# Kernel tuning notes

Measured on AMD Instinct MI355X. Metric: run time of the kernel, lower is better.

## Reference

```python
import jax, jax.numpy as jnp
import numpy as np

CROP = 48
THRESHOLD = 0.5
IOU_THRESHOLD = 0.5


def _conv(x, w, b):
    # x: [N,H,W,C], w: [kh,kw,Cin,Cout]
    y = jax.lax.conv_general_dilated(x, w, (1, 1), 'VALID',
                                     dimension_numbers=('NHWC', 'HWIO', 'NHWC'))
    return y + b


def _prelu(x, a):
    # a broadcasts over the channel-last axis
    return jnp.where(x >= 0, x, a * x)


def _maxpool(x, k, s, p):
    return jax.lax.reduce_window(x, -jnp.inf, jax.lax.max,
                                 (1, k, k, 1), (1, s, s, 1),
                                 ((0, 0), (p, p), (p, p), (0, 0)))


def _nms_keep(boxes, scores, valid, iou_thr):
    # fixed-shape greedy NMS (torchvision semantics: suppress iou > thr)
    N = boxes.shape[0]
    s = jnp.where(valid, scores, -jnp.inf)
    order = jnp.argsort(-s)
    b = boxes[order]
    x1, y1, x2, y2 = b[:, 0], b[:, 1], b[:, 2], b[:, 3]
    area = (x2 - x1) * (y2 - y1)
    xx1 = jnp.maximum(x1[:, None], x1[None, :])
    yy1 = jnp.maximum(y1[:, None], y1[None, :])
    xx2 = jnp.minimum(x2[:, None], x2[None, :])
    yy2 = jnp.minimum(y2[:, None], y2[None, :])
    inter = jnp.clip(xx2 - xx1, 0.0) * jnp.clip(yy2 - yy1, 0.0)
    iou = inter / (area[:, None] + area[None, :] - inter + 1e-12)
    keep0 = valid[order]
    idx = jnp.arange(N)

    def body(i, keep):
        sup = (iou[i] > iou_thr) & (idx > i) & keep[i] & keep
        return keep & ~sup

    keep_sorted = jax.lax.fori_loop(0, N, body, keep0)
    return jnp.zeros(N, bool).at[order].set(keep_sorted)


def setup_inputs() -> dict:
    key = jax.random.key(0)
    ks = jax.random.split(key, 24)
    H = W = 1024
    N = 2048
    image = jax.random.uniform(ks[0], (H, W, 3), jnp.float32) * 255.0
    x1 = jax.random.uniform(ks[1], (N,), jnp.float32) * (W - 130)
    y1 = jax.random.uniform(ks[2], (N,), jnp.float32) * (H - 130)
    bw = 20.0 + jax.random.uniform(ks[3], (N,), jnp.float32) * 100.0
    bh = 20.0 + jax.random.uniform(ks[4], (N,), jnp.float32) * 100.0
    bboxes = jnp.stack([x1, y1, x1 + bw, y1 + bh], axis=1)
    rn = lambda k, sh, s: jax.random.normal(k, sh, jnp.float32) * s
    return {
        'bboxes': bboxes, 'image': image,
        'conv1_w': rn(ks[5], (3, 3, 3, 32), 0.05), 'conv1_b': rn(ks[6], (32,), 0.01),
        'prelu1': 0.25 * jnp.ones((32,), jnp.float32),
        'conv2_w': rn(ks[7], (3, 3, 32, 64), 0.05), 'conv2_b': rn(ks[8], (64,), 0.01),
        'prelu2': 0.25 * jnp.ones((64,), jnp.float32),
        'conv3_w': rn(ks[9], (3, 3, 64, 64), 0.05), 'conv3_b': rn(ks[10], (64,), 0.01),
        'prelu3': 0.25 * jnp.ones((64,), jnp.float32),
        'conv4_w': rn(ks[11], (2, 2, 64, 128), 0.05), 'conv4_b': rn(ks[12], (128,), 0.01),
        'prelu4': 0.25 * jnp.ones((128,), jnp.float32),
        'fc5_w': rn(ks[13], (256, 1152), 0.02), 'fc5_b': rn(ks[14], (256,), 0.01),
        'prelu5': 0.25 * jnp.ones((256,), jnp.float32),
        'fc6a_w': rn(ks[15], (2, 256), 0.1), 'fc6a_b': rn(ks[16], (2,), 0.01),
        'fc6b_w': rn(ks[17], (4, 256), 0.1), 'fc6b_b': rn(ks[18], (4,), 0.01),
    }


def reference(bboxes, image, conv1_w, conv1_b, prelu1, conv2_w, conv2_b, prelu2,
              conv3_w, conv3_b, prelu3, conv4_w, conv4_b, prelu4,
              fc5_w, fc5_b, prelu5, fc6a_w, fc6a_b, fc6b_w, fc6b_b):
    H, W = image.shape[0], image.shape[1]
    N = bboxes.shape[0]
    # preprocess (torch: (x - 127.5) * 0.0078125)
    data = (image - 127.5) * 0.0078125  # [H,W,3]
    # clip boxes in place like the torch forward
    bx1 = jnp.clip(bboxes[:, 0], 0.0, None)
    by1 = jnp.clip(bboxes[:, 1], 0.0, None)
    bx2 = jnp.clip(bboxes[:, 2], None, float(W))
    by2 = jnp.clip(bboxes[:, 3], None, float(H))
    bb = jnp.stack([bx1, by1, bx2, by2], axis=1)  # clipped boxes [N,4]
    # integer crop windows (torch .int() truncation; coords >= 0)
    ib = bb.astype(jnp.int32)
    cw = jnp.maximum(ib[:, 2] - ib[:, 0], 1)
    ch = jnp.maximum(ib[:, 3] - ib[:, 1], 1)
    # nearest-neighbor resize to 48x48 (F.interpolate default mode='nearest')
    r = jnp.arange(CROP, dtype=jnp.int32)
    xs = ib[:, 0:1] + (r[None, :] * cw[:, None]) // CROP  # [N,48]
    ys = ib[:, 1:2] + (r[None, :] * ch[:, None]) // CROP  # [N,48]
    crops = data[ys[:, :, None], xs[:, None, :], :]  # [N,48,48,3] gather
    # CNN trunk
    h = _maxpool(_prelu(_conv(crops, conv1_w, conv1_b), prelu1), 3, 2, 1)
    h = _maxpool(_prelu(_conv(h, conv2_w, conv2_b), prelu2), 3, 2, 0)
    h = _maxpool(_prelu(_conv(h, conv3_w, conv3_b), prelu3), 2, 2, 0)
    h = _prelu(_conv(h, conv4_w, conv4_b), prelu4)  # [N,3,3,128]
    h = jnp.transpose(h, (0, 3, 1, 2)).reshape(N, -1)  # NCHW flatten like torch -> [N,1152]
    h = _prelu(h @ fc5_w.T + fc5_b, prelu5)  # [N,256]
    cls = jax.nn.softmax(h @ fc6a_w.T + fc6a_b, axis=1)  # [N,2]
    reg = h @ fc6b_w.T + fc6b_b  # [N,4]
    score = cls[:, 1]
    valid = score >= THRESHOLD
    w = bb[:, 2] - bb[:, 0]
    hgt = bb[:, 3] - bb[:, 1]
    out = jnp.stack([bb[:, 0] + reg[:, 0] * w,
                     bb[:, 1] + reg[:, 1] * hgt,
                     bb[:, 2] + reg[:, 2] * w,
                     bb[:, 3] + reg[:, 3] * hgt], axis=1)  # [N,4]
    keep = _nms_keep(out, score, valid, IOU_THRESHOLD)
    return jnp.where(keep[:, None], out, 0.0)
```

## Files before the change

### kernel.cpp

```cpp
#include <hip/hip_runtime.h>
#include <math.h>
#include <stdint.h>

#define NBOX 2048

#define P1_RS 25
#define P1_CS 576
#define P1_SZ 18432

__device__ __forceinline__ void fma4(float4& a, float s, const float4& w) {
  a.x = fmaf(s, w.x, a.x); a.y = fmaf(s, w.y, a.y);
  a.z = fmaf(s, w.z, a.z); a.w = fmaf(s, w.w, a.w);
}
__device__ __forceinline__ float4 max4(float4 a, float4 b) {
  return make_float4(fmaxf(a.x,b.x), fmaxf(a.y,b.y), fmaxf(a.z,b.z), fmaxf(a.w,b.w));
}
__device__ __forceinline__ float4 max34(float4 a, float4 b, float4 c) {
  return max4(max4(a, b), c);
}
__device__ __forceinline__ float4 prelu4(float4 v, float4 a) {
  float4 r;
  r.x = v.x >= 0.f ? v.x : a.x*v.x;
  r.y = v.y >= 0.f ? v.y : a.y*v.y;
  r.z = v.z >= 0.f ? v.z : a.z*v.z;
  r.w = v.w >= 0.f ? v.w : a.w*v.w;
  return r;
}
__device__ __forceinline__ float4 shfl4(float4 v, int src) {
  float4 r;
  r.x = __shfl(v.x, src, 64); r.y = __shfl(v.y, src, 64);
  r.z = __shfl(v.z, src, 64); r.w = __shfl(v.w, src, 64);
  return r;
}

__global__ __launch_bounds__(256) void k1_crop_conv1(
    const float* __restrict__ bboxes, const float* __restrict__ image,
    const float* __restrict__ w1, const float* __restrict__ b1, const float* __restrict__ a1,
    float* __restrict__ p1ws, int box0)
{
  __shared__ float crop[48*48*3];
  __shared__ float w1s[27*32];
  __shared__ float b1s[32], a1s[32];
  const int tid = threadIdx.x;
  const int n = box0 + blockIdx.x;

  for (int idx = tid; idx < 27*32; idx += 256) w1s[idx] = w1[idx];
  if (tid < 32) { b1s[tid] = b1[tid]; a1s[tid] = a1[tid]; }

  float f0 = bboxes[n*4+0], f1 = bboxes[n*4+1], f2 = bboxes[n*4+2], f3 = bboxes[n*4+3];
  float bx1 = fmaxf(f0, 0.f), by1 = fmaxf(f1, 0.f);
  float bx2 = fminf(f2, 1024.f), by2 = fminf(f3, 1024.f);
  int ix1 = (int)bx1, iy1 = (int)by1, ix2 = (int)bx2, iy2 = (int)by2;
  int cw = ix2 - ix1; if (cw < 1) cw = 1;
  int ch = iy2 - iy1; if (ch < 1) ch = 1;

  for (int idx = tid; idx < 6912; idx += 256) {
    int c = idx % 3; int t = idx / 3; int j = t % 48; int i = t / 48;
    int gx = ix1 + (j * cw) / 48;
    int gy = iy1 + (i * ch) / 48;
    float v = image[(gy*1024 + gx)*3 + c];
    crop[idx] = (v - 127.5f) * 0.0078125f;
  }
  __syncthreads();

  float* p1o = p1ws + (size_t)blockIdx.x * P1_SZ;

  for (int slot = tid; slot < 1104; slot += 256) {
    int cq = slot & 7;
    int t2 = slot >> 3;
    int pjq = t2 % 6;
    int pi  = t2 / 6;
    int pj0 = pjq * 4;
    int c0 = 2*pj0 - 1;
    float4 bias  = *(const float4*)&b1s[cq*4];
    float4 alpha = *(const float4*)&a1s[cq*4];
    float4 mx[4];
#pragma unroll
    for (int t = 0; t < 4; t++) mx[t] = make_float4(-3.0e38f,-3.0e38f,-3.0e38f,-3.0e38f);

#pragma unroll
    for (int dr = 0; dr < 3; dr++) {
      int r = 2*pi - 1 + dr;
      if (r < 0 || r > 45) continue;
      float4 acc[9];
#pragma unroll
      for (int c = 0; c < 9; c++) acc[c] = bias;
#pragma unroll
      for (int kh = 0; kh < 3; kh++) {
        int row = r + kh;
        float s[33];
#pragma unroll
        for (int d = 0; d < 11; d++) {
          int cc = c0 + d; cc = cc < 0 ? 0 : (cc > 47 ? 47 : cc);
          int base = row*144 + cc*3;
          s[d*3+0] = crop[base+0];
          s[d*3+1] = crop[base+1];
          s[d*3+2] = crop[base+2];
        }
#pragma unroll
        for (int kw = 0; kw < 3; kw++) {
#pragma unroll
          for (int ci = 0; ci < 3; ci++) {
            float4 w = *(const float4*)&w1s[((kh*3+kw)*3+ci)*32 + cq*4];
#pragma unroll
            for (int c = 0; c < 9; c++) fma4(acc[c], s[(c+kw)*3+ci], w);
          }
        }
      }
#pragma unroll
      for (int c = 0; c < 9; c++) {
        int cabs = c0 + c;
        if (cabs < 0 || cabs > 45) continue;
        float4 pv = prelu4(acc[c], alpha);
#pragma unroll
        for (int t = 0; t < 4; t++) {
          if (c >= 2*t && c <= 2*t+2) mx[t] = max4(mx[t], pv);
        }
      }
    }
#pragma unroll
    for (int t = 0; t < 4; t++) {
      int pj = pj0 + t;
      if (pj < 23) {
        int base = pi*P1_RS + pj;
        p1o[(cq*4+0)*P1_CS + base] = mx[t].x;
        p1o[(cq*4+1)*P1_CS + base] = mx[t].y;
        p1o[(cq*4+2)*P1_CS + base] = mx[t].z;
        p1o[(cq*4+3)*P1_CS + base] = mx[t].w;
      }
    }
  }
}

#define K2_LOADW(W, CI, KH) { \
  const float* wp_ = w2 + (((KH)*3)*32 + (CI))*64 + co0; \
  W[0] = *(const float4*)(wp_);            W[1] = *(const float4*)(wp_ + 4); \
  W[2] = *(const float4*)(wp_ + 2048);     W[3] = *(const float4*)(wp_ + 2052); \
  W[4] = *(const float4*)(wp_ + 4096);     W[5] = *(const float4*)(wp_ + 4100); }

#define K2_COMP(W, CIL, KH) { \
  const float* ip_ = &in_s[(CIL)*P1_CS + (rl+(KH))*P1_RS + j0]; \
  float s_[9]; \
  _Pragma("unroll") for (int d_ = 0; d_ < 9; d_++) s_[d_] = ip_[d_]; \
  _Pragma("unroll") for (int kw_ = 0; kw_ < 3; kw_++) { \
    _Pragma("unroll") for (int jj_ = 0; jj_ < 7; jj_++) { \
      fma4(acc[jj_][0], s_[jj_+kw_], W[kw_*2]); \
      fma4(acc[jj_][1], s_[jj_+kw_], W[kw_*2+1]); } } }

#define K2_STORE8(PJ, LO, HI) { \
  float* d_ = p2o + (size_t)co0*120 + pi*12 + (PJ); \
  float4 lo_ = (LO), hi_ = (HI); \
  d_[0]   = lo_.x; d_[120] = lo_.y; d_[240] = lo_.z; d_[360] = lo_.w; \
  d_[480] = hi_.x; d_[600] = hi_.y; d_[720] = hi_.z; d_[840] = hi_.w; }

__global__ __launch_bounds__(512, 4) void k2_conv2(
    const float* __restrict__ w2, const float* __restrict__ b2, const float* __restrict__ a2,
    const float* __restrict__ p1ws, float* __restrict__ p2ws)
{
  __shared__ float in_s[9216];
  const int tid = threadIdx.x;
  const float* p1o = p1ws + (size_t)blockIdx.x * P1_SZ;
  float* p2o = p2ws + (size_t)blockIdx.x * 7680;

  const int wav = __builtin_amdgcn_readfirstlane(tid >> 6);
  const int lane = tid & 63;
  int jt = lane / 21;
  int rl = lane - jt * 21;
  if (lane == 63) { jt = 2; rl = 20; }
  const int j0 = jt * 7;
  const int co0 = wav * 8;

  float4 bL = *(const float4*)&b2[co0];
  float4 bH = *(const float4*)&b2[co0+4];
  float4 aL = *(const float4*)&a2[co0];
  float4 aH = *(const float4*)&a2[co0+4];

  float4 acc[7][2];
#pragma unroll
  for (int jj = 0; jj < 7; jj++) { acc[jj][0] = bL; acc[jj][1] = bH; }

#pragma unroll 1
  for (int h = 0; h < 2; h++) {
    __syncthreads();
    for (int i4 = tid; i4 < 2304; i4 += 512)
      *(float4*)&in_s[i4*4] = *(const float4*)&p1o[h*9216 + i4*4];
    __syncthreads();

    const int cb = h*16;
    float4 wA[6], wB[6];
    K2_LOADW(wA, cb+0, 0);
#pragma unroll 1
    for (int ci = 0; ci < 16; ci += 2) {
      K2_LOADW(wB, cb+ci, 1);
      K2_COMP(wA, ci, 0);
      K2_LOADW(wA, cb+ci, 2);
      K2_COMP(wB, ci, 1);
      K2_LOADW(wB, cb+ci+1, 0);
      K2_COMP(wA, ci, 2);
      K2_LOADW(wA, cb+ci+1, 1);
      K2_COMP(wB, ci+1, 0);
      K2_LOADW(wB, cb+ci+1, 2);
      K2_COMP(wA, ci+1, 1);
      if (ci + 2 < 16) K2_LOADW(wA, cb+ci+2, 0);
      K2_COMP(wB, ci+1, 2);
    }
  }

#pragma unroll
  for (int jj = 0; jj < 7; jj++) {
    acc[jj][0] = prelu4(acc[jj][0], aL);
    acc[jj][1] = prelu4(acc[jj][1], aH);
  }

#pragma unroll
  for (int jj = 0; jj < 7; jj++) {
#pragma unroll
    for (int h = 0; h < 2; h++) {
      float4 v = acc[jj][h];
      float4 d1 = shfl4(v, lane + 1);
      float4 d2 = shfl4(v, lane + 2);
      acc[jj][h] = max34(v, d1, d2);
    }
  }
  float4 r0[2], r1[2];
#pragma unroll
  for (int h = 0; h < 2; h++) {
    r0[h] = shfl4(acc[0][h], lane + 21);
    r1[h] = shfl4(acc[1][h], lane + 21);
  }

  if (((rl & 1) == 0) && rl <= 18) {
    const int pi = rl >> 1;
    if (jt == 0) {
      K2_STORE8(0, max34(acc[0][0],acc[1][0],acc[2][0]), max34(acc[0][1],acc[1][1],acc[2][1]));
      K2_STORE8(1, max34(acc[2][0],acc[3][0],acc[4][0]), max34(acc[2][1],acc[3][1],acc[4][1]));
      K2_STORE8(2, max34(acc[4][0],acc[5][0],acc[6][0]), max34(acc[4][1],acc[5][1],acc[6][1]));
      K2_STORE8(3, max34(acc[6][0],r0[0],r1[0]),          max34(acc[6][1],r0[1],r1[1]));
    } else if (jt == 1) {
      K2_STORE8(4, max34(acc[1][0],acc[2][0],acc[3][0]), max34(acc[1][1],acc[2][1],acc[3][1]));
      K2_STORE8(5, max34(acc[3][0],acc[4][0],acc[5][0]), max34(acc[3][1],acc[4][1],acc[5][1]));
      K2_STORE8(6, max34(acc[5][0],acc[6][0],r0[0]),     max34(acc[5][1],acc[6][1],r0[1]));
    } else {
      K2_STORE8(7, max34(acc[0][0],acc[1][0],acc[2][0]), max34(acc[0][1],acc[1][1],acc[2][1]));
      K2_STORE8(8, max34(acc[2][0],acc[3][0],acc[4][0]), max34(acc[2][1],acc[3][1],acc[4][1]));
      K2_STORE8(9, max34(acc[4][0],acc[5][0],acc[6][0]), max34(acc[4][1],acc[5][1],acc[6][1]));
    }
  }
}

#define K3_LOADW(W, CI, KH) { \
  const float* wp_ = w3 + (((KH)*3)*64 + (CI))*64 + co0; \
  W[0] = *(const float4*)(wp_);            W[1] = *(const float4*)(wp_ + 4); \
  W[2] = *(const float4*)(wp_ + 4096);     W[3] = *(const float4*)(wp_ + 4100); \
  W[4] = *(const float4*)(wp_ + 8192);     W[5] = *(const float4*)(wp_ + 8196); }

#define K3_COMP(W, CIL, KH) { \
  const float* ip_ = ibase + (CIL)*120 + (KH)*12; \
  float2 sA_ = *(const float2*)(ip_); \
  float2 sB_ = *(const float2*)(ip_ + 2); \
  float s_[4] = {sA_.x, sA_.y, sB_.x, sB_.y}; \
  _Pragma("unroll") for (int kw_ = 0; kw_ < 3; kw_++) { \
    _Pragma("unroll") for (int c_ = 0; c_ < 2; c_++) { \
      fma4(acc[c_][0], s_[c_+kw_], W[kw_*2]); \
      fma4(acc[c_][1], s_[c_+kw_], W[kw_*2+1]); } } }

__global__ __launch_bounds__(512, 4) void k3_conv3(
    const float* __restrict__ w3, const float* __restrict__ b3, const float* __restrict__ a3,
    const float* __restrict__ p2ws, float* __restrict__ p3ws)
{
  __shared__ float in_s[7696];
  const int tid = threadIdx.x;
  const float* p2o = p2ws + (size_t)(blockIdx.x*2) * 7680;
  float* p3o0 = p3ws + (size_t)(blockIdx.x*2) * 1024;

  const int wav = __builtin_amdgcn_readfirstlane(tid >> 6);
  const int lane = tid & 63;
  const int b  = lane >> 5;
  const int r  = (lane >> 2) & 7;
  const int cg = lane & 3;
  const int co0 = wav * 8;

  float4 bL = *(const float4*)&b3[co0];
  float4 bH = *(const float4*)&b3[co0+4];
  float4 aL = *(const float4*)&a3[co0];
  float4 aH = *(const float4*)&a3[co0+4];

  float4 acc[2][2];
  acc[0][0] = bL; acc[0][1] = bH; acc[1][0] = bL; acc[1][1] = bH;

  const float* ibase = &in_s[b*3848 + r*12 + cg*2];

#pragma unroll 1
  for (int h = 0; h < 2; h++) {
    __syncthreads();
    for (int i4 = tid; i4 < 1920; i4 += 512) {
      int bb = (i4 >= 960) ? 1 : 0;
      int k = i4 - bb*960;
      *(float4*)&in_s[bb*3848 + k*4] = *(const float4*)&p2o[(size_t)bb*7680 + h*3840 + k*4];
    }
    __syncthreads();

    const int cb = h*32;
    float4 wA[6], wB[6];
    K3_LOADW(wA, cb+0, 0);
#pragma unroll 1
    for (int ci = 0; ci < 32; ci += 2) {
      K3_LOADW(wB, cb+ci, 1);
      K3_COMP(wA, ci, 0);
      K3_LOADW(wA, cb+ci, 2);
      K3_COMP(wB, ci, 1);
      K3_LOADW(wB, cb+ci+1, 0);
      K3_COMP(wA, ci, 2);
      K3_LOADW(wA, cb+ci+1, 1);
      K3_COMP(wB, ci+1, 0);
      K3_LOADW(wB, cb+ci+1, 2);
      K3_COMP(wA, ci+1, 1);
      if (ci + 2 < 32) K3_LOADW(wA, cb+ci+2, 0);
      K3_COMP(wB, ci+1, 2);
    }
  }

  float4 hm[2];
#pragma unroll
  for (int h = 0; h < 2; h++) {
    float4 p0 = prelu4(acc[0][h], h ? aH : aL);
    float4 p1 = prelu4(acc[1][h], h ? aH : aL);
    hm[h] = max4(p0, p1);
  }
  float4 o[2];
#pragma unroll
  for (int h = 0; h < 2; h++) {
    float4 d = shfl4(hm[h], lane + 4);
    o[h] = max4(hm[h], d);
  }
  if ((r & 1) == 0) {
    const int pi = r >> 1;
    float* d = p3o0 + b*1024 + (size_t)co0*16 + pi*4 + cg;
    d[0]   = o[0].x; d[16]  = o[0].y; d[32]  = o[0].z; d[48]  = o[0].w;
    d[64]  = o[1].x; d[80]  = o[1].y; d[96]  = o[1].z; d[112] = o[1].w;
  }
}

#define K4_LOADW(W, CI) { \
  const float* wp_ = w4 + (CI)*128 + co0; \
  W[0] = *(const float4*)(wp_);           W[1] = *(const float4*)(wp_ + 4); \
  W[2] = *(const float4*)(wp_ + 8192);    W[3] = *(const float4*)(wp_ + 8196); \
  W[4] = *(const float4*)(wp_ + 16384);   W[5] = *(const float4*)(wp_ + 16388); \
  W[6] = *(const float4*)(wp_ + 24576);   W[7] = *(const float4*)(wp_ + 24580); }

#define K4_COMP(W, CI) { \
  const float* ip_ = base + (CI)*16; \
  float i00 = ip_[0], i01 = ip_[1], i10 = ip_[4], i11 = ip_[5]; \
  fma4(acc0, i00, W[0]); fma4(acc1, i00, W[1]); \
  fma4(acc0, i01, W[2]); fma4(acc1, i01, W[3]); \
  fma4(acc0, i10, W[4]); fma4(acc1, i10, W[5]); \
  fma4(acc0, i11, W[6]); fma4(acc1, i11, W[7]); }

__global__ __launch_bounds__(512) void k4_conv4(
    const float* __restrict__ w4, const float* __restrict__ b4, const float* __restrict__ a4,
    const float* __restrict__ p3ws, float* __restrict__ c4ws)
{
  __shared__ float p3s[4*1032];
  const int tid = threadIdx.x;
  const int bi0 = blockIdx.x * 4;

  for (int i4 = tid; i4 < 1024; i4 += 512) {
    int bb = i4 >> 8, k = i4 & 255;
    *(float4*)&p3s[bb*1032 + k*4] = *(const float4*)&p3ws[(size_t)(bi0+bb)*1024 + k*4];
  }
  __syncthreads();

  const int wav = __builtin_amdgcn_readfirstlane(tid >> 6);
  const int lane = tid & 63;
  const int bx = lane >> 4;
  const int sp = lane & 15;
  const bool act = sp < 9;
  const int sq = act ? sp : 8;
  const int r = sq / 3, c = sq - 3*r;
  const float* base = &p3s[bx*1032 + r*4 + c];
  float* c4o = c4ws + (size_t)(bi0+bx)*1152;

#pragma unroll 1
  for (int p = 0; p < 2; p++) {
    const int co0 = p*64 + wav*8;
    float4 bL = *(const float4*)&b4[co0];
    float4 bH = *(const float4*)&b4[co0+4];
    float4 aL = *(const float4*)&a4[co0];
    float4 aH = *(const float4*)&a4[co0+4];
    float4 acc0 = bL, acc1 = bH;

    float4 wA[8], wB[8];
    K4_LOADW(wA, 0);
#pragma unroll 1
    for (int ci = 0; ci < 64; ci += 2) {
      K4_LOADW(wB, ci+1);
      K4_COMP(wA, ci);
      if (ci + 2 < 64) K4_LOADW(wA, ci+2);
      K4_COMP(wB, ci+1);
    }

    if (act) {
      float4 p0 = prelu4(acc0, aL);
      float4 p1 = prelu4(acc1, aH);
      float* d = c4o + (size_t)co0*9 + sp;
      d[0]  = p0.x; d[9]  = p0.y; d[18] = p0.z; d[27] = p0.w;
      d[36] = p1.x; d[45] = p1.y; d[54] = p1.z; d[63] = p1.w;
    }
  }
}

__global__ __launch_bounds__(256) void k5_fc(
    const float* __restrict__ fc5w, const float* __restrict__ fc5b, const float* __restrict__ a5,
    const float* __restrict__ w6a, const float* __restrict__ b6a,
    const float* __restrict__ w6b, const float* __restrict__ b6b,
    const float* __restrict__ bboxes, const float* __restrict__ c4ws,
    float* __restrict__ ws_scores, float* __restrict__ ws_boxes, int box0)
{
  __shared__ float c4s[8*1152];
  __shared__ float hs[8*256];
  __shared__ float l6[8][6];
  __shared__ float b5s[256], a5s[256];
  const int tid = threadIdx.x;
  const int lb0 = blockIdx.x * 8;
  b5s[tid] = fc5b[tid]; a5s[tid] = a5[tid];
  for (int idx4 = tid; idx4 < 2304; idx4 += 256)
    *(float4*)&c4s[idx4*4] = *(const float4*)&c4ws[(size_t)lb0*1152 + idx4*4];
  __syncthreads();

  const int og = tid & 31, bl = tid >> 5;
  float acc[8] = {0,0,0,0,0,0,0,0};
  const float* cbase = &c4s[bl*1152];
  for (int k = 0; k < 1152; k += 4) {
    float4 a = *(const float4*)&cbase[k];
#pragma unroll
    for (int u = 0; u < 8; u++) {
      int o = og + 32*u;
      float4 w = *(const float4*)&fc5w[(size_t)o*1152 + k];
      acc[u] += a.x*w.x + a.y*w.y + a.z*w.z + a.w*w.w;
    }
  }
#pragma unroll
  for (int u = 0; u < 8; u++) {
    int o = og + 32*u;
    float h = acc[u] + b5s[o];
    h = h >= 0.f ? h : a5s[o]*h;
    hs[bl*256 + o] = h;
  }
  __syncthreads();
  if (tid < 48) {
    int b = tid / 6, oi = tid % 6;
    const float* w = (oi < 2) ? &w6a[oi*256] : &w6b[(oi-2)*256];
    float d = (oi < 2) ? b6a[oi] : b6b[oi-2];
    const float* hh = &hs[b*256];
    for (int k = 0; k < 256; k++) d += hh[k]*w[k];
    l6[b][oi] = d;
  }
  __syncthreads();
  if (tid < 8) {
    int n = box0 + lb0 + tid;
    float l0 = l6[tid][0], l1 = l6[tid][1];
    float m = fmaxf(l0, l1);
    float e0 = expf(l0-m), e1 = expf(l1-m);
    float score = e1/(e0+e1);
    float r0 = l6[tid][2], r1 = l6[tid][3], r2 = l6[tid][4], r3 = l6[tid][5];
    float f0 = bboxes[n*4+0], f1 = bboxes[n*4+1], f2 = bboxes[n*4+2], f3 = bboxes[n*4+3];
    float bx1 = fmaxf(f0, 0.f), by1 = fmaxf(f1, 0.f);
    float bx2 = fminf(f2, 1024.f), by2 = fminf(f3, 1024.f);
    float w_ = bx2-bx1, h_ = by2-by1;
    ws_scores[n] = score;
    float4 ob = make_float4(bx1 + r0*w_, by1 + r1*h_, bx2 + r2*w_, by2 + r3*h_);
    *(float4*)&ws_boxes[n*4] = ob;
  }
}

__global__ __launch_bounds__(1024) void k6a_sort(
    const float* __restrict__ ws_scores, const float* __restrict__ ws_boxes,
    int* __restrict__ sidx_ws, float* __restrict__ sbox_ws,
    float* __restrict__ area_ws, int* __restrict__ nv_ws)
{
  __shared__ float skey[2048];
  __shared__ int   sidx[2048];
  const int tid = threadIdx.x;
  for (int i = tid; i < 2048; i += 1024) {
    float s = ws_scores[i];
    skey[i] = (s >= 0.5f) ? s : -INFINITY;
    sidx[i] = i;
  }
  __syncthreads();
  for (int k = 2; k <= 2048; k <<= 1) {
    for (int j = k >> 1; j > 0; j >>= 1) {
      for (int i = tid; i < 2048; i += 1024) {
        int ixj = i ^ j;
        if (ixj > i) {
          float a = skey[i], b = skey[ixj];
          int ia = sidx[i], ib = sidx[ixj];
          bool up = ((i & k) == 0);
          bool aAfterB = (a < b) || (a == b && ia > ib);
          if (up ? aAfterB : !aAfterB) {
            skey[i] = b; skey[ixj] = a; sidx[i] = ib; sidx[ixj] = ia;
          }
        }
      }
      __syncthreads();
    }
  }
  if (tid == 0) nv_ws[0] = 2048;
  __syncthreads();
  for (int i = tid; i < 2048; i += 1024) {
    if (skey[i] == -INFINITY && (i == 0 || skey[i-1] != -INFINITY)) nv_ws[0] = i;
    int n = sidx[i];
    sidx_ws[i] = n;
    float4 b = *(const float4*)&ws_boxes[n*4];
    *(float4*)&sbox_ws[i*4] = b;
    area_ws[i] = (b.z-b.x)*(b.w-b.y);
  }
}

__global__ __launch_bounds__(256) void k6b_iou(
    const int* __restrict__ nv_ws, const float* __restrict__ sbox_ws,
    const float* __restrict__ area_ws, unsigned long long* __restrict__ M)
{
  const int nv = nv_ws[0];
  int gt = blockIdx.x*256 + threadIdx.x;
  for (int w = gt; w < 2048*32; w += 128*256) {
    int i = w >> 5, wg = w & 31;
    if (i >= nv) continue;
    float4 bi = *(const float4*)&sbox_ws[i*4];
    float ai = area_ws[i];
    unsigned long long m = 0;
    int jbase = wg*64;
    if (jbase + 63 > i) {
      for (int jj = 0; jj < 64; jj++) {
        int j = jbase + jj;
        if (j <= i) continue;
        float4 bj = *(const float4*)&sbox_ws[j*4];
        float xx1 = fmaxf(bi.x, bj.x), yy1 = fmaxf(bi.y, bj.y);
        float xx2 = fminf(bi.z, bj.z), yy2 = fminf(bi.w, bj.w);
        float iw = fmaxf(xx2-xx1, 0.f), ih = fmaxf(yy2-yy1, 0.f);
        float inter = iw*ih;
        float iou = inter / (ai + area_ws[j] - inter + 1e-12f);
        if (iou > 0.5f) m |= (1ull << jj);
      }
    }
    M[w] = m;
  }
}

__global__ __launch_bounds__(1024) void k6c_scan(
    const int* __restrict__ nv_ws, const int* __restrict__ sidx_ws,
    const float* __restrict__ sbox_ws, const unsigned long long* __restrict__ M,
    float* __restrict__ out)
{
  __shared__ unsigned long long Msh[128*32];
  __shared__ unsigned long long rem_sh[32];
  const int tid = threadIdx.x;
  const int nv = nv_ws[0];
  unsigned long long rem = 0;

  for (int c0 = 0; c0 < 2048; c0 += 128) {
    if (c0 >= nv) break;
    for (int w = tid; w < 128*32; w += 1024) {
      int i = c0 + (w >> 5);
      if (i < nv) Msh[w] = M[(size_t)i*32 + (w & 31)];
    }
    __syncthreads();
    if (tid < 64) {
      int iend = c0 + 128; if (iend > nv) iend = nv;
      for (int i = c0; i < iend; i += 4) {
        unsigned long long m0=0, m1=0, m2=0, m3=0;
        int base = (i - c0) << 5;
        if (tid < 32) {
          m0 = Msh[base + tid];
          if (i+1 < iend) m1 = Msh[base + 32 + tid];
          if (i+2 < iend) m2 = Msh[base + 64 + tid];
          if (i+3 < iend) m3 = Msh[base + 96 + tid];
        }
        unsigned long long rw = __shfl(rem, (i >> 6), 64);
        if (!((rw >> (i & 63)) & 1ull)) rem |= m0;
        if (i+1 < iend) {
          rw = __shfl(rem, ((i+1) >> 6), 64);
          if (!((rw >> ((i+1) & 63)) & 1ull)) rem |= m1;
        }
        if (i+2 < iend) {
          rw = __shfl(rem, ((i+2) >> 6), 64);
          if (!((rw >> ((i+2) & 63)) & 1ull)) rem |= m2;
        }
        if (i+3 < iend) {
          rw = __shfl(rem, ((i+3) >> 6), 64);
          if (!((rw >> ((i+3) & 63)) & 1ull)) rem |= m3;
        }
      }
    }
    __syncthreads();
  }
  if (tid < 32) rem_sh[tid] = rem;
  __syncthreads();
  for (int i = tid; i < 2048; i += 1024) {
    bool keep = (i < nv) && !((rem_sh[i >> 6] >> (i & 63)) & 1ull);
    int n = sidx_ws[i];
    float4 b = *(const float4*)&sbox_ws[i*4];
    float4 o = keep ? b : make_float4(0.f,0.f,0.f,0.f);
    *(float4*)&out[n*4] = o;
  }
}

extern "C" void kernel_launch(void* const* d_in, const int* in_sizes, int n_in,
                              void* d_out, int out_size, void* d_ws, size_t ws_size,
                              hipStream_t stream)
{
  const float* bboxes = (const float*)d_in[0];
  const float* image  = (const float*)d_in[1];
  const float* w1 = (const float*)d_in[2];  const float* b1 = (const float*)d_in[3];  const float* a1 = (const float*)d_in[4];
  const float* w2 = (const float*)d_in[5];  const float* b2 = (const float*)d_in[6];  const float* a2 = (const float*)d_in[7];
  const float* w3 = (const float*)d_in[8];  const float* b3 = (const float*)d_in[9];  const float* a3 = (const float*)d_in[10];
  const float* w4 = (const float*)d_in[11]; const float* b4 = (const float*)d_in[12]; const float* a4 = (const float*)d_in[13];
  const float* fc5w = (const float*)d_in[14]; const float* fc5b = (const float*)d_in[15]; const float* a5 = (const float*)d_in[16];
  const float* w6a = (const float*)d_in[17]; const float* b6a = (const float*)d_in[18];
  const float* w6b = (const float*)d_in[19]; const float* b6b = (const float*)d_in[20];
  float* out = (float*)d_out;

  char* ws = (char*)d_ws;
  size_t off = 0;
  auto alloc = [&](size_t bytes) -> size_t {
    size_t p = off; off += (bytes + 255) & ~(size_t)255; return p;
  };
  size_t o_scores = alloc(NBOX*4);
  size_t o_boxes  = alloc(NBOX*16);
  size_t o_sidx   = alloc(NBOX*4);
  size_t o_sbox   = alloc(NBOX*16);
  size_t o_area   = alloc(NBOX*4);
  size_t o_nv     = alloc(256);
  size_t o_M      = alloc((size_t)NBOX*32*8);
  size_t fixed = off;
  const size_t perbox = (size_t)(P1_SZ + 7680 + 1024 + 1152) * 4;

  int B = NBOX;
  if (fixed + (size_t)B*perbox > ws_size) {
    size_t avail = ws_size > fixed ? ws_size - fixed : 0;
    B = (int)(avail / perbox);
    B &= ~7;
    if (B < 8) B = 8;
    if (B > NBOX) B = NBOX;
  }
  size_t o_p1 = alloc((size_t)B*P1_SZ*4);
  size_t o_p2 = alloc((size_t)B*7680*4);
  size_t o_p3 = alloc((size_t)B*1024*4);
  size_t o_c4 = alloc((size_t)B*1152*4);

  float* ws_scores = (float*)(ws + o_scores);
  float* ws_boxes  = (float*)(ws + o_boxes);
  int*   sidxp     = (int*)(ws + o_sidx);
  float* sboxp     = (float*)(ws + o_sbox);
  float* areap     = (float*)(ws + o_area);
  int*   nvp       = (int*)(ws + o_nv);
  unsigned long long* Mp = (unsigned long long*)(ws + o_M);
  float* p1p = (float*)(ws + o_p1);
  float* p2p = (float*)(ws + o_p2);
  float* p3p = (float*)(ws + o_p3);
  float* c4p = (float*)(ws + o_c4);

  for (int c0 = 0; c0 < NBOX; c0 += B) {
    int Bc = NBOX - c0; if (Bc > B) Bc = B;
    k1_crop_conv1<<<Bc, 256, 0, stream>>>(bboxes, image, w1, b1, a1, p1p, c0);
    k2_conv2<<<Bc, 512, 0, stream>>>(w2, b2, a2, p1p, p2p);
    k3_conv3<<<Bc/2, 512, 0, stream>>>(w3, b3, a3, p2p, p3p);
    k4_conv4<<<Bc/4, 512, 0, stream>>>(w4, b4, a4, p3p, c4p);
    k5_fc<<<Bc/8, 256, 0, stream>>>(fc5w, fc5b, a5, w6a, b6a, w6b, b6b,
                                    bboxes, c4p, ws_scores, ws_boxes, c0);
  }
  k6a_sort<<<1, 1024, 0, stream>>>(ws_scores, ws_boxes, sidxp, sboxp, areap, nvp);
  k6b_iou<<<128, 256, 0, stream>>>(nvp, sboxp, areap, Mp);
  k6c_scan<<<1, 1024, 0, stream>>>(nvp, sidxp, sboxp, Mp, out);
}
```

Baseline: 1.673 ms.

## Force weight loads through vector memory and simplify weight prefetch loops

Adds an opaque zero added to the weight base pointers in conv2/conv3/conv4 so the compiler cannot prove the address is wave-uniform. Weight loads then go through vector global loads instead of scalar loads. The software double-buffered weight prefetch in those kernels is replaced with simpler per-iteration loads. Conv1 drops its LDS staging of weights, bias and alpha and reads them straight from global memory. The aim is lower scalar-cache pressure and register use, at the cost of more vector memory traffic and less explicit load/compute overlap.

```diff
diff --git a/kernel.cpp b/kernel.cpp
--- a/kernel.cpp
+++ b/kernel.cpp
@@ -7,6 +7,10 @@
 #define P1_RS 25
 #define P1_CS 576
 #define P1_SZ 18432
+
+__device__ __forceinline__ int vzero() {
+  int z; asm volatile("v_mov_b32 %0, 0" : "=v"(z)); return z;
+}
 
 __device__ __forceinline__ void fma4(float4& a, float s, const float4& w) {
   a.x = fmaf(s, w.x, a.x); a.y = fmaf(s, w.y, a.y);
@@ -39,13 +43,8 @@
     float* __restrict__ p1ws, int box0)
 {
   __shared__ float crop[48*48*3];
-  __shared__ float w1s[27*32];
-  __shared__ float b1s[32], a1s[32];
   const int tid = threadIdx.x;
   const int n = box0 + blockIdx.x;
-
-  for (int idx = tid; idx < 27*32; idx += 256) w1s[idx] = w1[idx];
-  if (tid < 32) { b1s[tid] = b1[tid]; a1s[tid] = a1[tid]; }
 
   float f0 = bboxes[n*4+0], f1 = bboxes[n*4+1], f2 = bboxes[n*4+2], f3 = bboxes[n*4+3];
   float bx1 = fmaxf(f0, 0.f), by1 = fmaxf(f1, 0.f);
@@ -72,8 +71,8 @@
     int pi  = t2 / 6;
     int pj0 = pjq * 4;
     int c0 = 2*pj0 - 1;
-    float4 bias  = *(const float4*)&b1s[cq*4];
-    float4 alpha = *(const float4*)&a1s[cq*4];
+    float4 bias  = *(const float4*)&b1[cq*4];
+    float4 alpha = *(const float4*)&a1[cq*4];
     float4 mx[4];
 #pragma unroll
     for (int t = 0; t < 4; t++) mx[t] = make_float4(-3.0e38f,-3.0e38f,-3.0e38f,-3.0e38f);
@@ -101,7 +100,7 @@
         for (int kw = 0; kw < 3; kw++) {
 #pragma unroll
           for (int ci = 0; ci < 3; ci++) {
-            float4 w = *(const float4*)&w1s[((kh*3+kw)*3+ci)*32 + cq*4];
+            float4 w = *(const float4*)&w1[((kh*3+kw)*3+ci)*32 + cq*4];
 #pragma unroll
             for (int c = 0; c < 9; c++) fma4(acc[c], s[(c+kw)*3+ci], w);
           }
@@ -133,7 +132,7 @@
 }
 
 #define K2_LOADW(W, CI, KH) { \
-  const float* wp_ = w2 + (((KH)*3)*32 + (CI))*64 + co0; \
+  const float* wp_ = w2z + (((KH)*3)*32 + (CI))*64 + co0; \
   W[0] = *(const float4*)(wp_);            W[1] = *(const float4*)(wp_ + 4); \
   W[2] = *(const float4*)(wp_ + 2048);     W[3] = *(const float4*)(wp_ + 2052); \
   W[4] = *(const float4*)(wp_ + 4096);     W[5] = *(const float4*)(wp_ + 4100); }
@@ -161,6 +160,7 @@
   const int tid = threadIdx.x;
   const float* p1o = p1ws + (size_t)blockIdx.x * P1_SZ;
   float* p2o = p2ws + (size_t)blockIdx.x * 7680;
+  const float* w2z = w2 + vzero();
 
   const int wav = __builtin_amdgcn_readfirstlane(tid >> 6);
   const int lane = tid & 63;
@@ -187,22 +187,15 @@
     __syncthreads();
 
     const int cb = h*16;
-    float4 wA[6], wB[6];
-    K2_LOADW(wA, cb+0, 0);
 #pragma unroll 1
-    for (int ci = 0; ci < 16; ci += 2) {
-      K2_LOADW(wB, cb+ci, 1);
-      K2_COMP(wA, ci, 0);
-      K2_LOADW(wA, cb+ci, 2);
-      K2_COMP(wB, ci, 1);
-      K2_LOADW(wB, cb+ci+1, 0);
-      K2_COMP(wA, ci, 2);
-      K2_LOADW(wA, cb+ci+1, 1);
-      K2_COMP(wB, ci+1, 0);
-      K2_LOADW(wB, cb+ci+1, 2);
-      K2_COMP(wA, ci+1, 1);
-      if (ci + 2 < 16) K2_LOADW(wA, cb+ci+2, 0);
-      K2_COMP(wB, ci+1, 2);
+    for (int ci = 0; ci < 16; ci++) {
+      float4 w0[6], w1r[6], w2r[6];
+      K2_LOADW(w0, cb+ci, 0);
+      K2_LOADW(w1r, cb+ci, 1);
+      K2_COMP(w0, ci, 0);
+      K2_LOADW(w2r, cb+ci, 2);
+      K2_COMP(w1r, ci, 1);
+      K2_COMP(w2r, ci, 2);
     }
   }
 
@@ -249,7 +242,7 @@
 }
 
 #define K3_LOADW(W, CI, KH) { \
-  const float* wp_ = w3 + (((KH)*3)*64 + (CI))*64 + co0; \
+  const float* wp_ = w3z + (((KH)*3)*64 + (CI))*64 + co0; \
   W[0] = *(const float4*)(wp_);            W[1] = *(const float4*)(wp_ + 4); \
   W[2] = *(const float4*)(wp_ + 4096);     W[3] = *(const float4*)(wp_ + 4100); \
   W[4] = *(const float4*)(wp_ + 8192);     W[5] = *(const float4*)(wp_ + 8196); }
@@ -272,6 +265,7 @@
   const int tid = threadIdx.x;
   const float* p2o = p2ws + (size_t)(blockIdx.x*2) * 7680;
   float* p3o0 = p3ws + (size_t)(blockIdx.x*2) * 1024;
+  const float* w3z = w3 + vzero();
 
   const int wav = __builtin_amdgcn_readfirstlane(tid >> 6);
   const int lane = tid & 63;
@@ -301,22 +295,15 @@
     __syncthreads();
 
     const int cb = h*32;
-    float4 wA[6], wB[6];
-    K3_LOADW(wA, cb+0, 0);
 #pragma unroll 1
-    for (int ci = 0; ci < 32; ci += 2) {
-      K3_LOADW(wB, cb+ci, 1);
-      K3_COMP(wA, ci, 0);
-      K3_LOADW(wA, cb+ci, 2);
-      K3_COMP(wB, ci, 1);
-      K3_LOADW(wB, cb+ci+1, 0);
-      K3_COMP(wA, ci, 2);
-      K3_LOADW(wA, cb+ci+1, 1);
-      K3_COMP(wB, ci+1, 0);
-      K3_LOADW(wB, cb+ci+1, 2);
-      K3_COMP(wA, ci+1, 1);
-      if (ci + 2 < 32) K3_LOADW(wA, cb+ci+2, 0);
-      K3_COMP(wB, ci+1, 2);
+    for (int ci = 0; ci < 32; ci++) {
+      float4 w0[6], w1r[6], w2r[6];
+      K3_LOADW(w0, cb+ci, 0);
+      K3_LOADW(w1r, cb+ci, 1);
+      K3_COMP(w0, ci, 0);
+      K3_LOADW(w2r, cb+ci, 2);
+      K3_COMP(w1r, ci, 1);
+      K3_COMP(w2r, ci, 2);
     }
   }
 
@@ -342,7 +329,7 @@
 }
 
 #define K4_LOADW(W, CI) { \
-  const float* wp_ = w4 + (CI)*128 + co0; \
+  const float* wp_ = w4z + (CI)*128 + co0; \
   W[0] = *(const float4*)(wp_);           W[1] = *(const float4*)(wp_ + 4); \
   W[2] = *(const float4*)(wp_ + 8192);    W[3] = *(const float4*)(wp_ + 8196); \
   W[4] = *(const float4*)(wp_ + 16384);   W[5] = *(const float4*)(wp_ + 16388); \
@@ -363,6 +350,7 @@
   __shared__ float p3s[4*1032];
   const int tid = threadIdx.x;
   const int bi0 = blockIdx.x * 4;
+  const float* w4z = w4 + vzero();
 
   for (int i4 = tid; i4 < 1024; i4 += 512) {
     int bb = i4 >> 8, k = i4 & 255;
@@ -389,13 +377,12 @@
     float4 aH = *(const float4*)&a4[co0+4];
     float4 acc0 = bL, acc1 = bH;
 
-    float4 wA[8], wB[8];
-    K4_LOADW(wA, 0);
 #pragma unroll 1
     for (int ci = 0; ci < 64; ci += 2) {
+      float4 wA[8], wB[8];
+      K4_LOADW(wA, ci);
       K4_LOADW(wB, ci+1);
       K4_COMP(wA, ci);
-      if (ci + 2 < 64) K4_LOADW(wA, ci+2);
       K4_COMP(wB, ci+1);
     }
 
```

After: 1.852 ms. 1.11x slower.

## Restructure FC5 into coalesced warp-split dot products and read conv1 weights directly

Applied to the files above, without the earlier changes.

In the FC5 kernel, each half-wave of 32 lanes now computes one output neuron for one box. The lanes stride across the 1152-long row with coalesced float4 loads and combine partial sums with shuffle reductions, and the block grows to 512 threads. Before, each thread read a whole weight row with a large stride, which gave uncoalesced global access. Conv1 also drops its shared-memory staging of weights, bias and alpha and reads them straight from global memory, relying on the cache. In exchange, each box block now rereads the full fc5 weight matrix through a sequential loop over 128 outputs with shuffle overhead, and the conv1 inner loop now issues global loads.

```diff
diff --git a/kernel.cpp b/kernel.cpp
--- a/kernel.cpp
+++ b/kernel.cpp
@@ -39,13 +39,8 @@
     float* __restrict__ p1ws, int box0)
 {
   __shared__ float crop[48*48*3];
-  __shared__ float w1s[27*32];
-  __shared__ float b1s[32], a1s[32];
   const int tid = threadIdx.x;
   const int n = box0 + blockIdx.x;
-
-  for (int idx = tid; idx < 27*32; idx += 256) w1s[idx] = w1[idx];
-  if (tid < 32) { b1s[tid] = b1[tid]; a1s[tid] = a1[tid]; }
 
   float f0 = bboxes[n*4+0], f1 = bboxes[n*4+1], f2 = bboxes[n*4+2], f3 = bboxes[n*4+3];
   float bx1 = fmaxf(f0, 0.f), by1 = fmaxf(f1, 0.f);
@@ -72,8 +67,8 @@
     int pi  = t2 / 6;
     int pj0 = pjq * 4;
     int c0 = 2*pj0 - 1;
-    float4 bias  = *(const float4*)&b1s[cq*4];
-    float4 alpha = *(const float4*)&a1s[cq*4];
+    float4 bias  = *(const float4*)&b1[cq*4];
+    float4 alpha = *(const float4*)&a1[cq*4];
     float4 mx[4];
 #pragma unroll
     for (int t = 0; t < 4; t++) mx[t] = make_float4(-3.0e38f,-3.0e38f,-3.0e38f,-3.0e38f);
@@ -101,7 +96,7 @@
         for (int kw = 0; kw < 3; kw++) {
 #pragma unroll
           for (int ci = 0; ci < 3; ci++) {
-            float4 w = *(const float4*)&w1s[((kh*3+kw)*3+ci)*32 + cq*4];
+            float4 w = *(const float4*)&w1[((kh*3+kw)*3+ci)*32 + cq*4];
 #pragma unroll
             for (int c = 0; c < 9; c++) fma4(acc[c], s[(c+kw)*3+ci], w);
           }
@@ -409,7 +404,7 @@
   }
 }
 
-__global__ __launch_bounds__(256) void k5_fc(
+__global__ __launch_bounds__(512) void k5_fc(
     const float* __restrict__ fc5w, const float* __restrict__ fc5b, const float* __restrict__ a5,
     const float* __restrict__ w6a, const float* __restrict__ b6a,
     const float* __restrict__ w6b, const float* __restrict__ b6b,
@@ -419,41 +414,54 @@
   __shared__ float c4s[8*1152];
   __shared__ float hs[8*256];
   __shared__ float l6[8][6];
-  __shared__ float b5s[256], a5s[256];
   const int tid = threadIdx.x;
   const int lb0 = blockIdx.x * 8;
-  b5s[tid] = fc5b[tid]; a5s[tid] = a5[tid];
-  for (int idx4 = tid; idx4 < 2304; idx4 += 256)
+  for (int idx4 = tid; idx4 < 2304; idx4 += 512)
     *(float4*)&c4s[idx4*4] = *(const float4*)&c4ws[(size_t)lb0*1152 + idx4*4];
   __syncthreads();
 
-  const int og = tid & 31, bl = tid >> 5;
-  float acc[8] = {0,0,0,0,0,0,0,0};
-  const float* cbase = &c4s[bl*1152];
-  for (int k = 0; k < 1152; k += 4) {
-    float4 a = *(const float4*)&cbase[k];
-#pragma unroll
-    for (int u = 0; u < 8; u++) {
-      int o = og + 32*u;
-      float4 w = *(const float4*)&fc5w[(size_t)o*1152 + k];
-      acc[u] += a.x*w.x + a.y*w.y + a.z*w.z + a.w*w.w;
-    }
-  }
-#pragma unroll
-  for (int u = 0; u < 8; u++) {
-    int o = og + 32*u;
-    float h = acc[u] + b5s[o];
-    h = h >= 0.f ? h : a5s[o]*h;
-    hs[bl*256 + o] = h;
-  }
-  __syncthreads();
+  const int wav = __builtin_amdgcn_readfirstlane(tid >> 6);
+  const int lane = tid & 63;
+  const int half = lane >> 5;
+  const int l32  = lane & 31;
+  const int b    = 2*(wav & 3) + half;
+  const int ob   = (wav >> 2) * 128;
+  const float* cb = &c4s[b*1152 + l32*4];
+
+#pragma unroll 1
+  for (int oi = 0; oi < 128; oi++) {
+    const int o = ob + oi;
+    const float* wr = fc5w + (size_t)o*1152 + l32*4;
+    float acc = 0.f;
+#pragma unroll
+    for (int j = 0; j < 9; j++) {
+      float4 wv = *(const float4*)(wr + j*128);
+      float4 cv = *(const float4*)(cb + j*128);
+      acc = fmaf(cv.x, wv.x, acc);
+      acc = fmaf(cv.y, wv.y, acc);
+      acc = fmaf(cv.z, wv.z, acc);
+      acc = fmaf(cv.w, wv.w, acc);
+    }
+    acc += __shfl_down(acc, 16, 32);
+    acc += __shfl_down(acc,  8, 32);
+    acc += __shfl_down(acc,  4, 32);
+    acc += __shfl_down(acc,  2, 32);
+    acc += __shfl_down(acc,  1, 32);
+    if (l32 == 0) {
+      float h = acc + fc5b[o];
+      h = h >= 0.f ? h : a5[o]*h;
+      hs[b*256 + o] = h;
+    }
+  }
+  __syncthreads();
+
   if (tid < 48) {
-    int b = tid / 6, oi = tid % 6;
+    int bb = tid / 6, oi = tid % 6;
     const float* w = (oi < 2) ? &w6a[oi*256] : &w6b[(oi-2)*256];
     float d = (oi < 2) ? b6a[oi] : b6b[oi-2];
-    const float* hh = &hs[b*256];
+    const float* hh = &hs[bb*256];
     for (int k = 0; k < 256; k++) d += hh[k]*w[k];
-    l6[b][oi] = d;
+    l6[bb][oi] = d;
   }
   __syncthreads();
   if (tid < 8) {
@@ -468,8 +476,8 @@
     float bx2 = fminf(f2, 1024.f), by2 = fminf(f3, 1024.f);
     float w_ = bx2-bx1, h_ = by2-by1;
     ws_scores[n] = score;
-    float4 ob = make_float4(bx1 + r0*w_, by1 + r1*h_, bx2 + r2*w_, by2 + r3*h_);
-    *(float4*)&ws_boxes[n*4] = ob;
+    float4 ob2 = make_float4(bx1 + r0*w_, by1 + r1*h_, bx2 + r2*w_, by2 + r3*h_);
+    *(float4*)&ws_boxes[n*4] = ob2;
   }
 }
 
@@ -665,7 +673,7 @@
     k2_conv2<<<Bc, 512, 0, stream>>>(w2, b2, a2, p1p, p2p);
     k3_conv3<<<Bc/2, 512, 0, stream>>>(w3, b3, a3, p2p, p3p);
     k4_conv4<<<Bc/4, 512, 0, stream>>>(w4, b4, a4, p3p, c4p);
-    k5_fc<<<Bc/8, 256, 0, stream>>>(fc5w, fc5b, a5, w6a, b6a, w6b, b6b,
+    k5_fc<<<Bc/8, 512, 0, stream>>>(fc5w, fc5b, a5, w6a, b6a, w6b, b6b,
                                     bboxes, c4p, ws_scores, ws_boxes, c0);
   }
   k6a_sort<<<1, 1024, 0, stream>>>(ws_scores, ws_boxes, sidxp, sboxp, areap, nvp);
```

After: 1.552 ms (median of 2 runs). -7.3%, faster.
